# Kernel tuning notes

Hardware: AMD Instinct MI355X
Metric: run time of the kernel (lower is better)

Reference implementation:

```python
import jax, jax.numpy as jnp
import numpy as np

TAU_RC = 0.02
TAU_REF = 0.002
V_TH = 1.0
EPS = 1e-7


def lif_rate(I):
    # LIF firing-rate nonlinearity: r = 1/(tau_ref - tau_rc*log1p(-v_th/I)) for I > v_th+eps else 0
    good = I > V_TH + EPS
    safe_I = jnp.where(good, I, V_TH + 1.0)  # avoid log1p of invalid values
    r = 1.0 / (TAU_REF - TAU_RC * jnp.log1p(-V_TH / safe_I))
    return jnp.where(good, r, 0.0)


def setup_inputs() -> dict:
    key = jax.random.key(0)
    kq, kk, kv, ke, kg, kb = jax.random.split(key, 6)
    B, H, T, D = 2, 16, 2048, 64
    block_size = 2048
    Q = jax.random.normal(kq, (B, H, T, D), dtype=jnp.float32)
    K = jax.random.normal(kk, (B, H, T, D), dtype=jnp.float32)
    V = jax.random.normal(kv, (B, H, T, D), dtype=jnp.float32)
    enc = jax.random.normal(ke, (H, block_size, D), dtype=jnp.float32)
    # F.normalize(enc, dim=-1, eps=1e-8): x / max(||x||, eps)
    norm = jnp.maximum(jnp.linalg.norm(enc, axis=-1, keepdims=True), 1e-8)
    enc_hat = enc / norm
    gain = jax.random.uniform(kg, (1, H, block_size, 1), dtype=jnp.float32) * 200.0
    bias = jax.random.uniform(kb, (1, H, block_size, 1), dtype=jnp.float32)
    return {"Q": Q, "K": K, "V": V, "enc_hat": enc_hat, "gain": gain, "bias": bias}


def reference(Q, K, V, enc_hat, gain, bias):
    B, H, T, D = Q.shape
    temperature = jnp.asarray(D ** 0.5, dtype=Q.dtype)
    E = enc_hat[:, :T, :]          # [H, T, D]
    G = gain[:, :, :T, :]          # [1, H, T, 1]
    BIAS = bias[:, :, :T, :]       # [1, H, T, 1]
    # scores against fixed encoders (K is unused, matching the original module)
    I = G * jnp.einsum('bhtd,hsd->bhts', Q, E) + BIAS   # [B, H, T, T]
    scores = lif_rate(I) / temperature
    causal = jnp.tril(jnp.ones((T, T), dtype=bool))[None, None]
    scores = jnp.where(causal, scores, -jnp.inf)
    attn = jax.nn.softmax(scores, axis=-1)
    return jnp.einsum('bhts,bhsd->bhtd', attn, V)
```

## Files before the change

kernel.cpp:

```cpp
#include <hip/hip_runtime.h>
#include <hip/hip_bf16.h>
#include <math.h>

constexpr int Bb = 2, Hh = 16, Tt = 2048;

typedef __attribute__((ext_vector_type(8))) _Float16 f16x8;
typedef __attribute__((ext_vector_type(8))) short bf16x8;
typedef __attribute__((ext_vector_type(4))) float f32x4;
typedef __attribute__((ext_vector_type(16))) float f32x16;
typedef __attribute__((ext_vector_type(4))) unsigned int u32x4;
typedef unsigned int u32;

__device__ __forceinline__ short f2bf(float x){ __hip_bfloat16 h = __float2bfloat16(x); return *(short*)&h; }
__device__ __forceinline__ int swze(int row, int e){ return row*64 + ((((e>>3) ^ (row&7))<<3) | (e&7)); }
__device__ __forceinline__ int swzg(int row, int e0){ return row*64 + ((((e0>>3) ^ (row&7))<<3)); }

__device__ __forceinline__ void gll16(const void* g, void* l){
  __builtin_amdgcn_global_load_lds((const __attribute__((address_space(1))) u32*)g,
                                   (__attribute__((address_space(3))) u32*)l, 16, 0, 0);
}
__device__ __forceinline__ u32 cvtpk(float lo, float hi){
  u32 d; asm("v_cvt_pk_bf16_f32 %0, %1, %2" : "=v"(d) : "v"(lo), "v"(hi)); return d;
}

__global__ __launch_bounds__(256) void prep_e(const float* __restrict__ E, char* __restrict__ Eimg){
  const float* src = E + (size_t)blockIdx.x * 4096;
  char* dst = Eimg + (size_t)blockIdx.x * 16384;
#pragma unroll
  for (int i = 0; i < 2; ++i) {
    const int gid = threadIdx.x + 256 * i;
    const int row = gid >> 3, gc = gid & 7;
    const float* s8 = src + row * 64 + gc * 8;
    float4 a = *(const float4*)s8;
    float4 c = *(const float4*)(s8 + 4);
    float v[8] = {a.x, a.y, a.z, a.w, c.x, c.y, c.z, c.w};
    f16x8 hv, lv;
#pragma unroll
    for (int k = 0; k < 8; ++k) {
      _Float16 hi = (_Float16)v[k];
      hv[k] = hi; lv[k] = (_Float16)(v[k] - (float)hi);
    }
    const int off = row * 128 + ((gc ^ (row & 7)) << 4);
    *(f16x8*)(dst + off) = hv;
    *(f16x8*)(dst + 8192 + off) = lv;
  }
}

__global__ __launch_bounds__(256) void prep_v(const float* __restrict__ V, char* __restrict__ Vimg){
  __shared__ __align__(16) short Tl[64 * 64];
  const int tid = threadIdx.x;
  const int j = blockIdx.x & 31, bh = blockIdx.x >> 5;
  const int s0 = j * 64;
  {
    const int r = tid >> 2, c0 = (tid & 3) * 16;
    const float* src = V + ((size_t)bh * Tt + s0 + r) * 64 + c0;
#pragma unroll
    for (int i = 0; i < 4; ++i) {
      float4 t4 = ((const float4*)src)[i];
      float vv[4] = {t4.x, t4.y, t4.z, t4.w};
#pragma unroll
      for (int k = 0; k < 4; ++k) Tl[swze(c0 + 4 * i + k, r)] = f2bf(vv[k]);
    }
  }
  __syncthreads();
  {
    const int d = tid >> 2, sg = (tid & 3) * 16;
    bf16x8 a = *(const bf16x8*)&Tl[swzg(d, sg)];
    bf16x8 b = *(const bf16x8*)&Tl[swzg(d, sg + 8)];
    char* dst = Vimg + (size_t)blockIdx.x * 8192;
    *(bf16x8*)(dst + (sg >> 3) * 1024 + d * 16)       = a;
    *(bf16x8*)(dst + ((sg >> 3) + 1) * 1024 + d * 16) = b;
  }
}

__global__ __launch_bounds__(256, 3) void lif_attn8(
    const float* __restrict__ Q, const float* __restrict__ gain, const float* __restrict__ bias,
    const char* __restrict__ Eimg, const char* __restrict__ Vimg, float* __restrict__ out)
{
  __shared__ __align__(16) char Eb[2][16384];
  __shared__ __align__(16) float LsS[128];

  const int tid = threadIdx.x, lane = tid & 63;
  const int l31 = lane & 31, hi2 = lane >> 5;
  const int w = tid >> 6, wc = w & 1, wr = w >> 1;
  const int bh = blockIdx.x & 31, tb = 31 - (blockIdx.x >> 5);
  const int b = bh >> 4, h = bh & 15, t0 = tb * 64;
  const int tg = t0 + 32 * wc + l31;

  const char* etile = Eimg + (size_t)(h * 32) * 16384;
  const char* vtile = Vimg + (size_t)(bh * 32) * 8192;

  f16x8 qh[4], ql[4];
  {
    const float* qp = Q + ((size_t)(b * Hh + h) * Tt + tg) * 64 + 8 * hi2;
#pragma unroll
    for (int kk = 0; kk < 4; ++kk) {
      const float* p0 = qp + 16 * kk;
      float4 a = *(const float4*)p0;
      float4 c = *(const float4*)(p0 + 4);
      float v[8] = {a.x, a.y, a.z, a.w, c.x, c.y, c.z, c.w};
#pragma unroll
      for (int k = 0; k < 8; ++k) {
        _Float16 hi = (_Float16)v[k];
        qh[kk][k] = hi; ql[kk][k] = (_Float16)(v[k] - (float)hi);
      }
    }
  }
  const float gt = gain[h * Tt + tg], bt = bias[h * Tt + tg];

  const int rS = 32 * wr + l31;
  const int eB = rS * 128 + ((hi2 ^ (rS & 7)) << 4);

  const int g8a = 4 * wr + hi2;
  const char* vp0 = vtile + g8a * 1024 + l31 * 16;
  const char* vp1 = vtile + g8a * 1024 + (32 + l31) * 16;
  const char* vp2 = vtile + (g8a + 2) * 1024 + l31 * 16;
  const char* vp3 = vtile + (g8a + 2) * 1024 + (32 + l31) * 16;

  f32x16 oacc0 = 0.f, oacc1 = 0.f;
  float lsum = 0.f;
  f32x16 sA, sB;
  bf16x8 vA[4], vB[4];

  auto STAGE_E = [&](int n, int buf) {
    const char* g = etile + (size_t)n * 16384 + tid * 16;
    char* l = &Eb[buf][0] + tid * 16;
#pragma unroll
    for (int c2 = 0; c2 < 4; ++c2) gll16(g + c2 * 4096, l + c2 * 4096);
  };
  auto SSTEP = [&](int buf, f32x16& acc) {
    const char* ec = &Eb[buf][0];
    acc = 0.f;
#pragma unroll
    for (int kk = 0; kk < 4; ++kk) {
      f16x8 eh = *(const f16x8*)(ec + (eB ^ (kk << 5)));
      f16x8 el = *(const f16x8*)(ec + 8192 + (eB ^ (kk << 5)));
      acc = __builtin_amdgcn_mfma_f32_32x32x16_f16(eh, qh[kk], acc, 0, 0, 0);
      acc = __builtin_amdgcn_mfma_f32_32x32x16_f16(el, qh[kk], acc, 0, 0, 0);
      acc = __builtin_amdgcn_mfma_f32_32x32x16_f16(eh, ql[kk], acc, 0, 0, 0);
    }
  };
  auto VLOAD = [&](int n, bf16x8* vv) {
    const size_t o = (size_t)n * 8192;
    vv[0] = *(const bf16x8*)(vp0 + o);
    vv[1] = *(const bf16x8*)(vp1 + o);
    vv[2] = *(const bf16x8*)(vp2 + o);
    vv[3] = *(const bf16x8*)(vp3 + o);
  };

  auto BODY = [&](int j, f32x16& cur, f32x16& nxt, bf16x8* vc, bf16x8* vn) {
    if (j + 2 <= tb) STAGE_E(j + 2, j & 1);
    if (j + 1 <= tb) { SSTEP((j + 1) & 1, nxt); VLOAD(j + 1, vn); }
    float p[16];
#pragma unroll
    for (int r = 0; r < 16; ++r) {
      const float I = fmaf(gt, cur[r], bt);
      const float L2 = __log2f((I - 1.0f) * __builtin_amdgcn_rcpf(I));
      const float den = fmaf(-0.013862944f, L2, 0.002f);
      const float rd = __builtin_amdgcn_rcpf(den);
      const float pv = __builtin_amdgcn_exp2f(fmaf(0.18033688f, rd, -90.169312f));
      p[r] = (I > 1.0f + 1e-7f) ? pv : 7.1892351e-28f;
    }
    if (j == tb) {
#pragma unroll
      for (int rq = 0; rq < 4; ++rq)
#pragma unroll
        for (int rr = 0; rr < 4; ++rr)
          if (32 * wr + 8 * rq + 4 * hi2 + rr > 32 * wc + l31) p[4 * rq + rr] = 0.f;
    }
#pragma unroll
    for (int r = 0; r < 16; ++r) lsum += p[r];
#pragma unroll
    for (int kp = 0; kp < 2; ++kp) {
      u32 x0 = cvtpk(p[8 * kp + 0], p[8 * kp + 1]);
      u32 x1 = cvtpk(p[8 * kp + 2], p[8 * kp + 3]);
      u32 y0 = cvtpk(p[8 * kp + 4], p[8 * kp + 5]);
      u32 y1 = cvtpk(p[8 * kp + 6], p[8 * kp + 7]);
      asm("v_permlane32_swap_b32 %0, %1" : "+v"(x0), "+v"(y0));
      asm("v_permlane32_swap_b32 %0, %1" : "+v"(x1), "+v"(y1));
      u32x4 af = {x0, x1, y0, y1};
      bf16x8 pa = *(bf16x8*)&af;
      oacc0 = __builtin_amdgcn_mfma_f32_32x32x16_bf16(pa, vc[2 * kp + 0], oacc0, 0, 0, 0);
      oacc1 = __builtin_amdgcn_mfma_f32_32x32x16_bf16(pa, vc[2 * kp + 1], oacc1, 0, 0, 0);
    }
    __syncthreads();
  };

  STAGE_E(0, 0);
  if (tb >= 1) STAGE_E(1, 1);
  VLOAD(0, vA);
  __syncthreads();
  SSTEP(0, sA);
  __syncthreads();

  int j = 0;
  for (;;) {
    BODY(j, sA, sB, vA, vB); if (j == tb) break; ++j;
    BODY(j, sB, sA, vB, vA); if (j == tb) break; ++j;
  }

  lsum += __shfl_xor(lsum, 32);
  if (lane < 32) LsS[wr * 64 + wc * 32 + l31] = lsum;
  __syncthreads();
  float* red = (float*)&Eb[0][0];
  if (wr == 1) {
#pragma unroll
    for (int rq = 0; rq < 4; ++rq)
#pragma unroll
      for (int rr = 0; rr < 4; ++rr) {
        const int tr = 8 * rq + 4 * hi2 + rr;
        red[wc * 2048 + tr * 64 + l31]      = oacc0[4 * rq + rr];
        red[wc * 2048 + tr * 64 + 32 + l31] = oacc1[4 * rq + rr];
      }
  }
  __syncthreads();
  if (wr == 0) {
    float* ob = out + ((size_t)(b * Hh + h) * Tt + t0 + 32 * wc) * 64;
#pragma unroll
    for (int rq = 0; rq < 4; ++rq) {
      const int tr0 = 8 * rq + 4 * hi2;
      f32x4 lt0 = *(const f32x4*)&LsS[wc * 32 + tr0];
      f32x4 lt1 = *(const f32x4*)&LsS[64 + wc * 32 + tr0];
#pragma unroll
      for (int rr = 0; rr < 4; ++rr) {
        const int tr = tr0 + rr;
        const float linv = __builtin_amdgcn_rcpf(lt0[rr] + lt1[rr]);
        const float o0 = oacc0[4 * rq + rr] + red[wc * 2048 + tr * 64 + l31];
        const float o1 = oacc1[4 * rq + rr] + red[wc * 2048 + tr * 64 + 32 + l31];
        ob[(size_t)tr * 64 + l31]      = o0 * linv;
        ob[(size_t)tr * 64 + 32 + l31] = o1 * linv;
      }
    }
  }
}

extern "C" void kernel_launch(void* const* d_in, const int* in_sizes, int n_in,
                              void* d_out, int out_size, void* d_ws, size_t ws_size,
                              hipStream_t stream) {
  const float* Q    = (const float*)d_in[0];
  const float* V    = (const float*)d_in[2];
  const float* E    = (const float*)d_in[3];
  const float* gain = (const float*)d_in[4];
  const float* bias = (const float*)d_in[5];
  float* out = (float*)d_out;

  constexpr size_t EIMG_BYTES = (size_t)Hh * 32 * 16384;
  char* Eimg = (char*)d_ws;
  char* Vimg = (char*)d_ws + EIMG_BYTES;

  prep_e<<<Hh * 32, 256, 0, stream>>>(E, Eimg);
  prep_v<<<Bb * Hh * 32, 256, 0, stream>>>(V, Vimg);
  lif_attn8<<<1024, 256, 0, stream>>>(Q, gain, bias, Eimg, Vimg, out);
}
```

Baseline: 74.00 us.

## Replace full syncthreads with partial vmcnt waits, setprio around MFMA, simplify LIF mask

Replaces __syncthreads in the main loop with an explicit s_waitcnt vmcnt(4) plus s_barrier, so the V register loads issued for the next step can stay in flight across the barrier. It adds sched_barrier fences and raises wave priority around the MFMA sections to encourage overlap between waves. The LIF validity select becomes a branch-free fabs/fmax clamp. The risks are wrong vmcnt counting, which could race with the global_load_lds staging of E, and the clamp giving different values for some invalid inputs.

```diff
diff --git a/kernel.cpp b/kernel.cpp
--- a/kernel.cpp
+++ b/kernel.cpp
@@ -73,7 +73,7 @@
   }
 }
 
-__global__ __launch_bounds__(256, 3) void lif_attn8(
+__global__ __launch_bounds__(256, 3) void lif_attn9(
     const float* __restrict__ Q, const float* __restrict__ gain, const float* __restrict__ bias,
     const char* __restrict__ Eimg, const char* __restrict__ Vimg, float* __restrict__ out)
 {
@@ -131,6 +131,7 @@
   auto SSTEP = [&](int buf, f32x16& acc) {
     const char* ec = &Eb[buf][0];
     acc = 0.f;
+    __builtin_amdgcn_s_setprio(1);
 #pragma unroll
     for (int kk = 0; kk < 4; ++kk) {
       f16x8 eh = *(const f16x8*)(ec + (eB ^ (kk << 5)));
@@ -139,6 +140,7 @@
       acc = __builtin_amdgcn_mfma_f32_32x32x16_f16(el, qh[kk], acc, 0, 0, 0);
       acc = __builtin_amdgcn_mfma_f32_32x32x16_f16(eh, ql[kk], acc, 0, 0, 0);
     }
+    __builtin_amdgcn_s_setprio(0);
   };
   auto VLOAD = [&](int n, bf16x8* vv) {
     const size_t o = (size_t)n * 8192;
@@ -150,16 +152,18 @@
 
   auto BODY = [&](int j, f32x16& cur, f32x16& nxt, bf16x8* vc, bf16x8* vn) {
     if (j + 2 <= tb) STAGE_E(j + 2, j & 1);
+    __builtin_amdgcn_sched_barrier(0);
     if (j + 1 <= tb) { SSTEP((j + 1) & 1, nxt); VLOAD(j + 1, vn); }
     float p[16];
 #pragma unroll
     for (int r = 0; r < 16; ++r) {
       const float I = fmaf(gt, cur[r], bt);
-      const float L2 = __log2f((I - 1.0f) * __builtin_amdgcn_rcpf(I));
+      const float a = (I - 1.0f) * __builtin_fabsf(__builtin_amdgcn_rcpf(I));
+      const float L2 = __log2f(a);
       const float den = fmaf(-0.013862944f, L2, 0.002f);
       const float rd = __builtin_amdgcn_rcpf(den);
       const float pv = __builtin_amdgcn_exp2f(fmaf(0.18033688f, rd, -90.169312f));
-      p[r] = (I > 1.0f + 1e-7f) ? pv : 7.1892351e-28f;
+      p[r] = fmaxf(pv, 7.1892351e-28f);
     }
     if (j == tb) {
 #pragma unroll
@@ -170,6 +174,7 @@
     }
 #pragma unroll
     for (int r = 0; r < 16; ++r) lsum += p[r];
+    __builtin_amdgcn_s_setprio(1);
 #pragma unroll
     for (int kp = 0; kp < 2; ++kp) {
       u32 x0 = cvtpk(p[8 * kp + 0], p[8 * kp + 1]);
@@ -183,20 +188,35 @@
       oacc0 = __builtin_amdgcn_mfma_f32_32x32x16_bf16(pa, vc[2 * kp + 0], oacc0, 0, 0, 0);
       oacc1 = __builtin_amdgcn_mfma_f32_32x32x16_bf16(pa, vc[2 * kp + 1], oacc1, 0, 0, 0);
     }
-    __syncthreads();
+    __builtin_amdgcn_s_setprio(0);
   };
 
   STAGE_E(0, 0);
   if (tb >= 1) STAGE_E(1, 1);
+  __builtin_amdgcn_sched_barrier(0);
   VLOAD(0, vA);
-  __syncthreads();
+  asm volatile("s_waitcnt vmcnt(4)" ::: "memory");
+  __builtin_amdgcn_s_barrier();
+  __builtin_amdgcn_sched_barrier(0);
   SSTEP(0, sA);
-  __syncthreads();
+  asm volatile("s_waitcnt vmcnt(4)" ::: "memory");
+  __builtin_amdgcn_s_barrier();
+  __builtin_amdgcn_sched_barrier(0);
 
   int j = 0;
   for (;;) {
-    BODY(j, sA, sB, vA, vB); if (j == tb) break; ++j;
-    BODY(j, sB, sA, vB, vA); if (j == tb) break; ++j;
+    BODY(j, sA, sB, vA, vB);
+    if (j == tb) break;
+    asm volatile("s_waitcnt vmcnt(4)" ::: "memory");
+    __builtin_amdgcn_s_barrier();
+    __builtin_amdgcn_sched_barrier(0);
+    ++j;
+    BODY(j, sB, sA, vB, vA);
+    if (j == tb) break;
+    asm volatile("s_waitcnt vmcnt(4)" ::: "memory");
+    __builtin_amdgcn_s_barrier();
+    __builtin_amdgcn_sched_barrier(0);
+    ++j;
   }
 
   lsum += __shfl_xor(lsum, 32);
@@ -250,5 +270,5 @@
 
   prep_e<<<Hh * 32, 256, 0, stream>>>(E, Eimg);
   prep_v<<<Bb * Hh * 32, 256, 0, stream>>>(V, Vimg);
-  lif_attn8<<<1024, 256, 0, stream>>>(Q, gain, bias, Eimg, Vimg, out);
-}
+  lif_attn9<<<1024, 256, 0, stream>>>(Q, gain, bias, Eimg, Vimg, out);
+}
```

Result: no change. 73.69 us (-0.4%).
